# Performance work log

Hardware: AMD Instinct MI355X
Metric: run time of the kernel (lower is better)

## Reference

```python
import jax, jax.numpy as jnp
import numpy as np

N_NODES = 100000
N_EDGES = 1600000
HIDDEN = 128
NUM_FEAT = 1
NUM_CLASSES = 10
NUM_GRAPHS = 512


def setup_inputs() -> dict:
    key = jax.random.key(0)
    ks = jax.random.split(key, 16)
    x = jax.random.normal(ks[0], (N_NODES, NUM_FEAT), dtype=jnp.float32)
    edge_index = jax.random.randint(ks[1], (2, N_EDGES), 0, N_NODES, dtype=jnp.int64)
    batch = jnp.sort(jax.random.randint(ks[2], (N_NODES,), 0, NUM_GRAPHS, dtype=jnp.int64))
    def glorot(k, shape):
        lim = float(np.sqrt(6.0 / (shape[0] + shape[1])))
        return jax.random.uniform(k, shape, jnp.float32, -lim, lim)
    params = {
        'W1': glorot(ks[3], (NUM_FEAT, HIDDEN)), 'b1': jnp.zeros((HIDDEN,), jnp.float32),
        'W2': glorot(ks[4], (HIDDEN, HIDDEN)), 'b2': jnp.zeros((HIDDEN,), jnp.float32),
        'W3': glorot(ks[5], (HIDDEN, HIDDEN)), 'b3': jnp.zeros((HIDDEN,), jnp.float32),
        'W4': glorot(ks[6], (HIDDEN, HIDDEN)), 'b4': jnp.zeros((HIDDEN,), jnp.float32),
        'W5': glorot(ks[7], (HIDDEN, HIDDEN)), 'b5': jnp.zeros((HIDDEN,), jnp.float32),
        'Wlin': glorot(ks[8], (HIDDEN, NUM_CLASSES)), 'blin': jnp.zeros((NUM_CLASSES,), jnp.float32),
    }
    return {'x': x, 'edge_index': edge_index, 'batch': batch, **params}


def _gcn_norm(edge_index, n_nodes):
    # PyG GCNConv: add self-loops, sym-normalize by deg^-1/2 on both ends.
    loops = jnp.arange(n_nodes, dtype=edge_index.dtype)
    src = jnp.concatenate([edge_index[0], loops])
    dst = jnp.concatenate([edge_index[1], loops])
    deg = jax.ops.segment_sum(jnp.ones_like(dst, jnp.float32), dst, num_segments=n_nodes)
    dis = jnp.where(deg > 0, jax.lax.rsqrt(jnp.maximum(deg, 1.0)), 0.0)
    norm = dis[src] * dis[dst]  # [E + N]
    return src, dst, norm


def _gcn_conv(h, W, b, src, dst, norm, n_nodes):
    h = h @ W  # transform first (PyG order)
    msg = h[src] * norm[:, None]  # gather + scale, [E+N, H]
    out = jax.ops.segment_sum(msg, dst, num_segments=n_nodes)  # scatter-add
    return out + b


def reference(x, edge_index, batch, W1, b1, W2, b2, W3, b3, W4, b4, W5, b5, Wlin, blin):
    n = x.shape[0]
    src, dst, norm = _gcn_norm(edge_index, n)
    h = _gcn_conv(x, W1, b1, src, dst, norm, n)
    h = _gcn_conv(h, W2, b2, src, dst, norm, n)
    h = _gcn_conv(h, W3, b3, src, dst, norm, n)
    h = _gcn_conv(h, W4, b4, src, dst, norm, n)
    h = _gcn_conv(h, W5, b5, src, dst, norm, n)
    # global mean pool over graphs
    sums = jax.ops.segment_sum(h, batch, num_segments=NUM_GRAPHS)
    cnts = jax.ops.segment_sum(jnp.ones((n,), jnp.float32), batch, num_segments=NUM_GRAPHS)
    pooled = sums / jnp.maximum(cnts, 1.0)[:, None]
    # dropout is identity at eval
    return pooled @ Wlin + blin
```

## Files before the change

### kernel.cpp

```cpp
#include <hip/hip_runtime.h>

#define NT 256
#define BN_SHIFT 8
#define NBUCKET_MAX 512
#define CAP 8192
#define EPB 4096

__global__ void __launch_bounds__(768)
prep_kernel(const float* __restrict__ W1, const float* __restrict__ b1,
            const float* __restrict__ W2, const float* __restrict__ b2,
            const float* __restrict__ W3, const float* __restrict__ b3,
            const float* __restrict__ W4, const float* __restrict__ b4,
            const float* __restrict__ W5, const float* __restrict__ b5,
            const float* __restrict__ Wlin, float* __restrict__ qout,
            int* __restrict__ gcur, int NB) {
  __shared__ float cur[6][128];
  const int tid = threadIdx.x;
  for (int i = tid; i < NB; i += 768) gcur[i] = 0;
  const int vi = tid >> 7;
  const int t = tid & 127;
  float init;
  if (vi == 0) init = W1[t];
  else if (vi == 1) init = b1[t];
  else if (vi == 2) init = b2[t];
  else if (vi == 3) init = b3[t];
  else if (vi == 4) init = b4[t];
  else init = b5[t];
  cur[vi][t] = init;
  __syncthreads();
  const float* Ws[4] = {W2, W3, W4, W5};
  #pragma unroll
  for (int l = 0; l < 4; ++l) {
    const int nact = l + 2;
    float s = 0.f;
    if (vi < nact) {
      const float* __restrict__ W = Ws[l];
      #pragma unroll 8
      for (int k = 0; k < 128; ++k) s += cur[vi][k] * W[k * 128 + t];
    }
    __syncthreads();
    if (vi < nact) cur[vi][t] = s;
    __syncthreads();
  }
  if (tid < 60) {
    int v = tid / 10, c = tid % 10;
    float s = 0.f;
    for (int k = 0; k < 128; ++k) s += cur[v][k] * Wlin[k * 10 + c];
    qout[v * 10 + c] = s;
  }
}

__global__ void binA_kernel(const int* __restrict__ ei, int* __restrict__ gcur,
                            unsigned int* __restrict__ dump, int E, int NB) {
  __shared__ unsigned int cnt[NBUCKET_MAX];
  __shared__ unsigned int base[NBUCKET_MAX];
  const int t = threadIdx.x;
  const int e0 = blockIdx.x * EPB;
  const bool vec_ok = ((E & 3) == 0);
  for (int b = t; b < NB; b += 256) cnt[b] = 0;
  __syncthreads();
  unsigned int slot[16];
  unsigned int dreg[16];
  #pragma unroll
  for (int jj = 0; jj < 4; ++jj) {
    int e = e0 + jj * 1024 + t * 4;
    if (vec_ok && e + 3 < E) {
      int4 d4 = *reinterpret_cast<const int4*>(&ei[E + e]);
      dreg[jj * 4 + 0] = (unsigned)d4.x;
      dreg[jj * 4 + 1] = (unsigned)d4.y;
      dreg[jj * 4 + 2] = (unsigned)d4.z;
      dreg[jj * 4 + 3] = (unsigned)d4.w;
      #pragma unroll
      for (int k = 0; k < 4; ++k)
        slot[jj * 4 + k] = atomicAdd(&cnt[dreg[jj * 4 + k] >> BN_SHIFT], 1u);
    } else {
      #pragma unroll
      for (int k = 0; k < 4; ++k) {
        int ee = e + k;
        if (ee < E) {
          unsigned d = (unsigned)ei[E + ee];
          dreg[jj * 4 + k] = d;
          slot[jj * 4 + k] = atomicAdd(&cnt[d >> BN_SHIFT], 1u);
        }
      }
    }
  }
  __syncthreads();
  for (int b = t; b < NB; b += 256) {
    unsigned int c = cnt[b];
    base[b] = c ? (unsigned int)atomicAdd(&gcur[b], (int)c) : 0u;
  }
  __syncthreads();
  #pragma unroll
  for (int jj = 0; jj < 4; ++jj) {
    int e = e0 + jj * 1024 + t * 4;
    unsigned s4v[4];
    bool fast = (vec_ok && e + 3 < E);
    if (fast) {
      int4 s4 = *reinterpret_cast<const int4*>(&ei[e]);
      s4v[0] = (unsigned)s4.x; s4v[1] = (unsigned)s4.y;
      s4v[2] = (unsigned)s4.z; s4v[3] = (unsigned)s4.w;
    }
    #pragma unroll
    for (int k = 0; k < 4; ++k) {
      int ee = e + k;
      if (ee < E) {
        unsigned s = fast ? s4v[k] : (unsigned)ei[ee];
        unsigned d = dreg[jj * 4 + k];
        unsigned b = d >> BN_SHIFT;
        unsigned pos = base[b] + slot[jj * 4 + k];
        if (pos < CAP)
          dump[(size_t)b * CAP + pos] = (s << BN_SHIFT) | (d & 255u);
      }
    }
  }
}

__global__ void binB_kernel(const unsigned int* __restrict__ dump,
                            const int* __restrict__ gcur,
                            const float* __restrict__ x, int* __restrict__ col,
                            int2* __restrict__ rl, float* __restrict__ dis2,
                            float* __restrict__ sq, float2* __restrict__ ta, int N) {
  __shared__ int cnt[256];
  __shared__ int sc[256];
  __shared__ int cur[256];
  const int b = blockIdx.x, t = threadIdx.x;
  cnt[t] = 0;
  __syncthreads();
  int total = gcur[b];
  if (total > CAP) total = CAP;
  const unsigned int* seg = dump + (size_t)b * CAP;
  unsigned wreg[CAP / 256];
  #pragma unroll
  for (int k = 0; k < CAP / 256; ++k) {
    int i = (k << 8) + t;
    if (i < total) {
      unsigned w = seg[i];
      wreg[k] = w;
      atomicAdd(&cnt[w & 255u], 1);
    }
  }
  __syncthreads();
  int v = cnt[t];
  sc[t] = v;
  __syncthreads();
  for (int off = 1; off < 256; off <<= 1) {
    int u = (t >= off) ? sc[t - off] : 0;
    __syncthreads();
    sc[t] += u;
    __syncthreads();
  }
  int rbase = b * CAP + sc[t] - v;
  cur[t] = rbase;
  __syncthreads();
  #pragma unroll
  for (int k = 0; k < CAP / 256; ++k) {
    int i = (k << 8) + t;
    if (i < total) {
      unsigned w = wreg[k];
      int slot = atomicAdd(&cur[w & 255u], 1);
      col[slot] = (int)(w >> BN_SHIFT);
    }
  }
  int node = (b << BN_SHIFT) + t;
  if (node < N) {
    rl[node] = make_int2(rbase, v);
    float dis = rsqrtf((float)v + 1.0f);
    dis2[node] = dis * dis;
    sq[node] = 1.0f / dis;
    ta[node] = make_float2(dis * x[node], dis);
  }
}

__global__ void gather_kernel(const int* __restrict__ col, const int2* __restrict__ rl,
                              const float* __restrict__ dis2,
                              const float2* __restrict__ tin, float2* __restrict__ tout,
                              float* __restrict__ ssave, int N) {
  int tid = blockIdx.x * blockDim.x + threadIdx.x;
  int node = tid >> 3, l8 = tid & 7;
  if (node >= N) return;
  int2 r = rl[node];
  float sx = 0.f, sy = 0.f;
  int j = l8;
  for (; j + 8 < r.y; j += 16) {
    int c0 = col[r.x + j];
    int c1 = col[r.x + j + 8];
    float2 a0 = tin[c0];
    float2 a1 = tin[c1];
    sx += a0.x + a1.x;
    sy += a0.y + a1.y;
  }
  if (j < r.y) {
    float2 a = tin[col[r.x + j]];
    sx += a.x;
    sy += a.y;
  }
  sx += __shfl_xor(sx, 1);
  sx += __shfl_xor(sx, 2);
  sx += __shfl_xor(sx, 4);
  sy += __shfl_xor(sy, 1);
  sy += __shfl_xor(sy, 2);
  sy += __shfl_xor(sy, 4);
  if (l8 == 0) {
    float2 ts = tin[node];
    float m = dis2[node];
    float oy = m * (sy + ts.y);
    tout[node] = make_float2(m * (sx + ts.x), oy);
    if (ssave) ssave[node] = oy;
  }
}

__device__ __forceinline__ int lower_bound_i(const int* a, int n, int key) {
  int lo = 0, hi = n;
  while (lo < hi) {
    int mid = (lo + hi) >> 1;
    if (a[mid] < key) lo = mid + 1; else hi = mid;
  }
  return lo;
}

__global__ void pool_kernel(const int* __restrict__ batch, int N,
                            const float2* __restrict__ t5, const float* __restrict__ s4,
                            const float* __restrict__ s3, const float* __restrict__ s2,
                            const float* __restrict__ s1, const float* __restrict__ sq,
                            const float* __restrict__ q, const float* __restrict__ blin,
                            float* __restrict__ out) {
  int g = blockIdx.x;
  __shared__ int sh[2];
  if (threadIdx.x == 0) {
    sh[0] = lower_bound_i(batch, N, g);
    sh[1] = lower_bound_i(batch, N, g + 1);
  }
  __syncthreads();
  int lo = sh[0], hi = sh[1];
  float a[5] = {0.f, 0.f, 0.f, 0.f, 0.f};
  for (int i = lo + threadIdx.x; i < hi; i += blockDim.x) {
    float qq = sq[i];
    a[0] += t5[i].x * qq;
    a[1] += s4[i] * qq;
    a[2] += s3[i] * qq;
    a[3] += s2[i] * qq;
    a[4] += s1[i] * qq;
  }
  __shared__ float red[4][5];
  __shared__ float m5[5];
  int lane = threadIdx.x & 63, wave = threadIdx.x >> 6;
  #pragma unroll
  for (int j = 0; j < 5; ++j)
    #pragma unroll
    for (int o = 32; o > 0; o >>= 1) a[j] += __shfl_down(a[j], o);
  if (lane == 0)
    #pragma unroll
    for (int j = 0; j < 5; ++j) red[wave][j] = a[j];
  __syncthreads();
  if (threadIdx.x == 0) {
    float denom = fmaxf((float)(hi - lo), 1.0f);
    #pragma unroll
    for (int j = 0; j < 5; ++j)
      m5[j] = (red[0][j] + red[1][j] + red[2][j] + red[3][j]) / denom;
  }
  __syncthreads();
  int t = threadIdx.x;
  if (t < 10) {
    out[g * 10 + t] = m5[0] * q[t] + m5[1] * q[10 + t] + m5[2] * q[20 + t] +
                      m5[3] * q[30 + t] + m5[4] * q[40 + t] + q[50 + t] + blin[t];
  }
}

extern "C" void kernel_launch(void* const* d_in, const int* in_sizes, int n_in,
                              void* d_out, int out_size, void* d_ws, size_t ws_size,
                              hipStream_t stream) {
  const float* x    = (const float*)d_in[0];
  const int*   ei   = (const int*)d_in[1];
  const int*   batch= (const int*)d_in[2];
  const float* W1   = (const float*)d_in[3];
  const float* b1   = (const float*)d_in[4];
  const float* W2   = (const float*)d_in[5];
  const float* b2   = (const float*)d_in[6];
  const float* W3   = (const float*)d_in[7];
  const float* b3   = (const float*)d_in[8];
  const float* W4   = (const float*)d_in[9];
  const float* b4   = (const float*)d_in[10];
  const float* W5   = (const float*)d_in[11];
  const float* b5   = (const float*)d_in[12];
  const float* Wlin = (const float*)d_in[13];
  const float* blin = (const float*)d_in[14];

  const int N  = in_sizes[0];
  const int E  = in_sizes[1] / 2;
  const int G  = out_size / 10;
  const int NB = (N + 255) >> BN_SHIFT;

  float* ws = (float*)d_ws;
  size_t off = 0;
  float2* ta   = (float2*)(ws + off); off += 2 * (size_t)N;
  float2* tb   = (float2*)(ws + off); off += 2 * (size_t)N;
  float*  dis2 = ws + off;            off += N;
  float*  sq   = ws + off;            off += N;
  float*  s1   = ws + off;            off += N;
  float*  s2   = ws + off;            off += N;
  float*  s3   = ws + off;            off += N;
  float*  s4   = ws + off;            off += N;
  float*  qv   = ws + off;            off += 64;
  if (off & 1) off++;
  int2* rl     = (int2*)(ws + off);   off += 2 * (size_t)N;
  int* gcur    = (int*)(ws + off);    off += NB;
  if (off & 1) off++;
  unsigned int* dump = (unsigned int*)(ws + off); off += (size_t)NB * CAP;
  int* col     = (int*)(ws + off);    off += (size_t)NB * CAP;
  (void)ws_size;

  const int gridA = (E + EPB - 1) / EPB;
  const int gridG = (8 * N + NT - 1) / NT;

  prep_kernel<<<1, 768, 0, stream>>>(W1, b1, W2, b2, W3, b3, W4, b4, W5, b5,
                                     Wlin, qv, gcur, NB);
  binA_kernel<<<gridA, 256, 0, stream>>>(ei, gcur, dump, E, NB);
  binB_kernel<<<NB, 256, 0, stream>>>(dump, gcur, x, col, rl, dis2, sq, ta, N);

  gather_kernel<<<gridG, NT, 0, stream>>>(col, rl, dis2, ta, tb, s1, N);
  gather_kernel<<<gridG, NT, 0, stream>>>(col, rl, dis2, tb, ta, s2, N);
  gather_kernel<<<gridG, NT, 0, stream>>>(col, rl, dis2, ta, tb, s3, N);
  gather_kernel<<<gridG, NT, 0, stream>>>(col, rl, dis2, tb, ta, s4, N);
  gather_kernel<<<gridG, NT, 0, stream>>>(col, rl, dis2, ta, tb, nullptr, N);

  pool_kernel<<<G, 256, 0, stream>>>(batch, N, tb, s4, s3, s2, s1, sq, qv, blin,
                                     (float*)d_out);
}
```

Baseline: 126.1 us.

## Fuse graph mean-pool partial sums into gather kernels via block-segmented atomics

Each gather layer now computes its pooled contribution (value times sq) and reduces it per graph inside the block, issuing atomicAdds into a small per-graph pooled buffer. This removes the per-layer ssave arrays and the heavy pool kernel that reread five N-sized arrays. The last layer also skips the unused y channel. Separately, EPB is halved to launch more binning blocks. Cost: an extra __syncthreads and a serial 32-element scan per block, plus float atomics that make the summation order nondeterministic.

```diff
diff --git a/kernel.cpp b/kernel.cpp
--- a/kernel.cpp
+++ b/kernel.cpp
@@ -4,7 +4,7 @@
 #define BN_SHIFT 8
 #define NBUCKET_MAX 512
 #define CAP 8192
-#define EPB 4096
+#define EPB 2048
 
 __global__ void __launch_bounds__(768)
 prep_kernel(const float* __restrict__ W1, const float* __restrict__ b1,
@@ -13,10 +13,11 @@
             const float* __restrict__ W4, const float* __restrict__ b4,
             const float* __restrict__ W5, const float* __restrict__ b5,
             const float* __restrict__ Wlin, float* __restrict__ qout,
-            int* __restrict__ gcur, int NB) {
+            int* __restrict__ gcur, int NB, float* __restrict__ pooled, int G) {
   __shared__ float cur[6][128];
   const int tid = threadIdx.x;
   for (int i = tid; i < NB; i += 768) gcur[i] = 0;
+  for (int i = tid; i < G * 5; i += 768) pooled[i] = 0.f;
   const int vi = tid >> 7;
   const int t = tid & 127;
   float init;
@@ -59,10 +60,10 @@
   const bool vec_ok = ((E & 3) == 0);
   for (int b = t; b < NB; b += 256) cnt[b] = 0;
   __syncthreads();
-  unsigned int slot[16];
-  unsigned int dreg[16];
-  #pragma unroll
-  for (int jj = 0; jj < 4; ++jj) {
+  unsigned int slot[8];
+  unsigned int dreg[8];
+  #pragma unroll
+  for (int jj = 0; jj < 2; ++jj) {
     int e = e0 + jj * 1024 + t * 4;
     if (vec_ok && e + 3 < E) {
       int4 d4 = *reinterpret_cast<const int4*>(&ei[E + e]);
@@ -92,7 +93,7 @@
   }
   __syncthreads();
   #pragma unroll
-  for (int jj = 0; jj < 4; ++jj) {
+  for (int jj = 0; jj < 2; ++jj) {
     int e = e0 + jj * 1024 + t * 4;
     unsigned s4v[4];
     bool fast = (vec_ok && e + 3 < E);
@@ -172,41 +173,81 @@
   }
 }
 
+template <bool LAST>
 __global__ void gather_kernel(const int* __restrict__ col, const int2* __restrict__ rl,
                               const float* __restrict__ dis2,
-                              const float2* __restrict__ tin, float2* __restrict__ tout,
-                              float* __restrict__ ssave, int N) {
+                              const float* __restrict__ sq,
+                              const int* __restrict__ batch,
+                              const float2* __restrict__ tin,
+                              float2* __restrict__ tout,
+                              float* __restrict__ pooled, int slot, int N) {
+  __shared__ float sval[32];
+  __shared__ int sg[32];
   int tid = blockIdx.x * blockDim.x + threadIdx.x;
   int node = tid >> 3, l8 = tid & 7;
-  if (node >= N) return;
-  int2 r = rl[node];
+  int nloc = threadIdx.x >> 3;
+  bool valid = (node < N);
   float sx = 0.f, sy = 0.f;
-  int j = l8;
-  for (; j + 8 < r.y; j += 16) {
-    int c0 = col[r.x + j];
-    int c1 = col[r.x + j + 8];
-    float2 a0 = tin[c0];
-    float2 a1 = tin[c1];
-    sx += a0.x + a1.x;
-    sy += a0.y + a1.y;
-  }
-  if (j < r.y) {
-    float2 a = tin[col[r.x + j]];
-    sx += a.x;
-    sy += a.y;
+  if (valid) {
+    int2 r = rl[node];
+    int j = l8;
+    for (; j + 8 < r.y; j += 16) {
+      int c0 = col[r.x + j];
+      int c1 = col[r.x + j + 8];
+      float2 a0 = tin[c0];
+      float2 a1 = tin[c1];
+      sx += a0.x + a1.x;
+      if (!LAST) sy += a0.y + a1.y;
+    }
+    if (j < r.y) {
+      float2 a = tin[col[r.x + j]];
+      sx += a.x;
+      if (!LAST) sy += a.y;
+    }
   }
   sx += __shfl_xor(sx, 1);
   sx += __shfl_xor(sx, 2);
   sx += __shfl_xor(sx, 4);
-  sy += __shfl_xor(sy, 1);
-  sy += __shfl_xor(sy, 2);
-  sy += __shfl_xor(sy, 4);
+  if (!LAST) {
+    sy += __shfl_xor(sy, 1);
+    sy += __shfl_xor(sy, 2);
+    sy += __shfl_xor(sy, 4);
+  }
   if (l8 == 0) {
-    float2 ts = tin[node];
-    float m = dis2[node];
-    float oy = m * (sy + ts.y);
-    tout[node] = make_float2(m * (sx + ts.x), oy);
-    if (ssave) ssave[node] = oy;
+    if (valid) {
+      float2 ts = tin[node];
+      float m = dis2[node];
+      float ox = m * (sx + ts.x);
+      float c;
+      if (LAST) {
+        c = ox * sq[node];
+      } else {
+        float oy = m * (sy + ts.y);
+        tout[node] = make_float2(ox, oy);
+        c = oy * sq[node];
+      }
+      sval[nloc] = c;
+      sg[nloc] = batch[node];
+    } else {
+      sval[nloc] = 0.f;
+      sg[nloc] = -1;
+    }
+  }
+  __syncthreads();
+  if (threadIdx.x == 0) {
+    float acc = sval[0];
+    int g = sg[0];
+    #pragma unroll 4
+    for (int i = 1; i < 32; ++i) {
+      if (sg[i] == g) {
+        acc += sval[i];
+      } else {
+        if (g >= 0) atomicAdd(&pooled[g * 5 + slot], acc);
+        g = sg[i];
+        acc = sval[i];
+      }
+    }
+    if (g >= 0) atomicAdd(&pooled[g * 5 + slot], acc);
   }
 }
 
@@ -219,51 +260,26 @@
   return lo;
 }
 
-__global__ void pool_kernel(const int* __restrict__ batch, int N,
-                            const float2* __restrict__ t5, const float* __restrict__ s4,
-                            const float* __restrict__ s3, const float* __restrict__ s2,
-                            const float* __restrict__ s1, const float* __restrict__ sq,
-                            const float* __restrict__ q, const float* __restrict__ blin,
-                            float* __restrict__ out) {
+__global__ void final_kernel(const int* __restrict__ batch, int N,
+                             const float* __restrict__ pooled,
+                             const float* __restrict__ q,
+                             const float* __restrict__ blin,
+                             float* __restrict__ out) {
   int g = blockIdx.x;
-  __shared__ int sh[2];
+  __shared__ int cntS;
   if (threadIdx.x == 0) {
-    sh[0] = lower_bound_i(batch, N, g);
-    sh[1] = lower_bound_i(batch, N, g + 1);
-  }
-  __syncthreads();
-  int lo = sh[0], hi = sh[1];
-  float a[5] = {0.f, 0.f, 0.f, 0.f, 0.f};
-  for (int i = lo + threadIdx.x; i < hi; i += blockDim.x) {
-    float qq = sq[i];
-    a[0] += t5[i].x * qq;
-    a[1] += s4[i] * qq;
-    a[2] += s3[i] * qq;
-    a[3] += s2[i] * qq;
-    a[4] += s1[i] * qq;
-  }
-  __shared__ float red[4][5];
-  __shared__ float m5[5];
-  int lane = threadIdx.x & 63, wave = threadIdx.x >> 6;
-  #pragma unroll
-  for (int j = 0; j < 5; ++j)
-    #pragma unroll
-    for (int o = 32; o > 0; o >>= 1) a[j] += __shfl_down(a[j], o);
-  if (lane == 0)
-    #pragma unroll
-    for (int j = 0; j < 5; ++j) red[wave][j] = a[j];
-  __syncthreads();
-  if (threadIdx.x == 0) {
-    float denom = fmaxf((float)(hi - lo), 1.0f);
-    #pragma unroll
-    for (int j = 0; j < 5; ++j)
-      m5[j] = (red[0][j] + red[1][j] + red[2][j] + red[3][j]) / denom;
+    int lo = lower_bound_i(batch, N, g);
+    int hi = lower_bound_i(batch, N, g + 1);
+    cntS = hi - lo;
   }
   __syncthreads();
   int t = threadIdx.x;
   if (t < 10) {
-    out[g * 10 + t] = m5[0] * q[t] + m5[1] * q[10 + t] + m5[2] * q[20 + t] +
-                      m5[3] * q[30 + t] + m5[4] * q[40 + t] + q[50 + t] + blin[t];
+    float inv = 1.0f / fmaxf((float)cntS, 1.0f);
+    const float* pg = &pooled[g * 5];
+    out[g * 10 + t] = (pg[0] * q[t] + pg[1] * q[10 + t] + pg[2] * q[20 + t] +
+                       pg[3] * q[30 + t] + pg[4] * q[40 + t]) * inv +
+                      q[50 + t] + blin[t];
   }
 }
 
@@ -297,10 +313,7 @@
   float2* tb   = (float2*)(ws + off); off += 2 * (size_t)N;
   float*  dis2 = ws + off;            off += N;
   float*  sq   = ws + off;            off += N;
-  float*  s1   = ws + off;            off += N;
-  float*  s2   = ws + off;            off += N;
-  float*  s3   = ws + off;            off += N;
-  float*  s4   = ws + off;            off += N;
+  float*  pooled = ws + off;          off += (size_t)G * 5;
   float*  qv   = ws + off;            off += 64;
   if (off & 1) off++;
   int2* rl     = (int2*)(ws + off);   off += 2 * (size_t)N;
@@ -314,16 +327,15 @@
   const int gridG = (8 * N + NT - 1) / NT;
 
   prep_kernel<<<1, 768, 0, stream>>>(W1, b1, W2, b2, W3, b3, W4, b4, W5, b5,
-                                     Wlin, qv, gcur, NB);
+                                     Wlin, qv, gcur, NB, pooled, G);
   binA_kernel<<<gridA, 256, 0, stream>>>(ei, gcur, dump, E, NB);
   binB_kernel<<<NB, 256, 0, stream>>>(dump, gcur, x, col, rl, dis2, sq, ta, N);
 
-  gather_kernel<<<gridG, NT, 0, stream>>>(col, rl, dis2, ta, tb, s1, N);
-  gather_kernel<<<gridG, NT, 0, stream>>>(col, rl, dis2, tb, ta, s2, N);
-  gather_kernel<<<gridG, NT, 0, stream>>>(col, rl, dis2, ta, tb, s3, N);
-  gather_kernel<<<gridG, NT, 0, stream>>>(col, rl, dis2, tb, ta, s4, N);
-  gather_kernel<<<gridG, NT, 0, stream>>>(col, rl, dis2, ta, tb, nullptr, N);
-
-  pool_kernel<<<G, 256, 0, stream>>>(batch, N, tb, s4, s3, s2, s1, sq, qv, blin,
-                                     (float*)d_out);
-}
+  gather_kernel<false><<<gridG, NT, 0, stream>>>(col, rl, dis2, sq, batch, ta, tb, pooled, 4, N);
+  gather_kernel<false><<<gridG, NT, 0, stream>>>(col, rl, dis2, sq, batch, tb, ta, pooled, 3, N);
+  gather_kernel<false><<<gridG, NT, 0, stream>>>(col, rl, dis2, sq, batch, ta, tb, pooled, 2, N);
+  gather_kernel<false><<<gridG, NT, 0, stream>>>(col, rl, dis2, sq, batch, tb, ta, pooled, 1, N);
+  gather_kernel<true ><<<gridG, NT, 0, stream>>>(col, rl, dis2, sq, batch, ta, nullptr, pooled, 0, N);
+
+  final_kernel<<<G, 64, 0, stream>>>(batch, N, pooled, qv, blin, (float*)d_out);
+}
```

New measurement: 157.3 us. +24.8%, slower.
